# Kernel optimization log

Measured on AMD Instinct MI355X. Metric: run time of the kernel, lower is better.

Reference implementation:

```python
import jax, jax.numpy as jnp
import numpy as np

D = 512      # bit dimension
M = 131072   # stored reference points
B = 64       # query batch (batchLength in source)
EPS = 1e-6


def setup_inputs() -> dict:
    key = jax.random.key(0)
    k1, k2, k3, k4, k5 = jax.random.split(key, 5)
    return {
        "t_X1_T_bits": jax.random.randint(k1, (D, B), 0, 2, dtype=jnp.int32),
        "t_X2_T_bits": jax.random.randint(k2, (D, M), 0, 2, dtype=jnp.int32),
        # block-packed copy used only by the original custom backward; ignored here
        "t_X2_byDimBlock_T_bits": jax.random.randint(k3, (16, 1024), 0, 2, dtype=jnp.int32),
        "t_Y_knn": jax.random.normal(k4, (M,), dtype=jnp.float32),
        "t_W": jax.random.uniform(k5, (D,), dtype=jnp.float32, minval=0.5, maxval=1.5),
        "alpha": jnp.zeros((), jnp.float32),
        "beta": jnp.ones((), jnp.float32),
        "k": jnp.asarray(0.1, jnp.float32),
        "j": jnp.asarray(0.1, jnp.float32),
    }


def _squash_F(x, k, j):
    # F() from kNNFit: two-stage rational squash
    inner = x * (1 - k) / (k * (1 - 2 * jnp.abs(x)) + 1)
    t = 2 * inner - 1
    return 0.5 + 0.5 * t * (1 + j) / (-j * (1 - 2 * jnp.abs(t)) + 1)


def reference(t_X1_T_bits, t_X2_T_bits, t_X2_byDimBlock_T_bits, t_Y_knn,
              t_W, alpha, beta, k, j):
    # Weighted Hamming distance between every stored point (X2, [D,M]) and
    # every query (X1, [D,B]):
    #   WHD[m,b] = sum_d W[d] * (x1[d,b] XOR x2[d,m])
    # For 0/1 bits: xor = x1 + x2 - 2*x1*x2, so WHD decomposes into two
    # weighted bit-counts plus one GEMM (avoids a [D,M,B] intermediate).
    X1 = t_X1_T_bits.astype(jnp.float32)  # [D,B]
    X2 = t_X2_T_bits.astype(jnp.float32)  # [D,M]
    s1 = t_W @ X1                                            # [B]
    s2 = t_W @ X2                                            # [M]
    cross = jnp.einsum('dm,db->mb', X2, t_W[:, None] * X1)   # [M,B]
    t_WHDx = s1[None, :] + s2[:, None] - 2.0 * cross         # [M,B]

    t_norm_W = jnp.sum(jnp.abs(t_W)) + EPS                   # L1 norm
    t_FQx = _squash_F(1.0 - t_WHDx / t_norm_W, k, j)         # [M,B]
    t_score = jnp.mean(t_FQx * t_Y_knn[:, None], axis=0)     # [B]
    return beta * (t_score + alpha)
```

## Files before the change

kernel.cpp:

```cpp
#include <hip/hip_runtime.h>
#include <hip/hip_bf16.h>


#define DD 512
#define MM 131072
#define BQ 64
#define NWG 1024
#define NWAVES (NWG * 4)
#define WS_BFRAG 0
#define WS_META  65536
#define WS_PART  131072

typedef __attribute__((ext_vector_type(8))) short short8;
typedef __attribute__((ext_vector_type(16))) float floatx16;
typedef __attribute__((ext_vector_type(4))) unsigned int uintx4;
typedef __attribute__((ext_vector_type(4))) int intx4;

__global__ __launch_bounds__(256) void knn_setup(
    const int* __restrict__ X1, const float* __restrict__ W,
    void* __restrict__ ws) {
  short8* bm = (short8*)((char*)ws + WS_BFRAG);
  float* meta = (float*)((char*)ws + WS_META);
  const int tid = threadIdx.x;
#pragma unroll
  for (int i = 0; i < 16; ++i) {
    const int e = tid + 256 * i;
    const int lane = e & 63, t = (e >> 6) & 1, s = e >> 7;
    const int half = lane >> 5, col = lane & 31;
    const int b = t * 32 + col;
    short8 f;
#pragma unroll
    for (int j = 0; j < 8; ++j) {
      const int d = s * 16 + half * 8 + j;
      unsigned short hb = __builtin_bit_cast(unsigned short, __float2bfloat16(W[d]));
      if (X1[d * BQ + b]) hb ^= 0x8000u;
      f[j] = (short)hb;
    }
    bm[e] = f;
  }
  __shared__ float s1p[4][64];
  const int chunk = tid >> 6, b = tid & 63;
  float s = 0.f;
  for (int d = chunk * 128; d < chunk * 128 + 128; ++d)
    s += W[d] * (float)X1[d * BQ + b];
  s1p[chunk][b] = s;
  __syncthreads();
  if (tid < 64) {
    meta[tid] = s1p[0][tid] + s1p[1][tid] + s1p[2][tid] + s1p[3][tid];
    float nw = 0.f;
#pragma unroll
    for (int j = 0; j < 8; ++j) nw += fabsf(W[tid * 8 + j]);
    nw += __shfl_xor(nw, 32);
    nw += __shfl_xor(nw, 16);
    nw += __shfl_xor(nw, 8);
    nw += __shfl_xor(nw, 4);
    nw += __shfl_xor(nw, 2);
    nw += __shfl_xor(nw, 1);
    if (tid == 0) meta[64] = 1.0f / (nw + 1e-6f);
  }
}

__global__ __launch_bounds__(256, 4) void knn_main(
    const int* __restrict__ X2, const float* __restrict__ Y,
    const float* __restrict__ kp, const float* __restrict__ jp,
    const void* __restrict__ ws_ro, float* __restrict__ partials) {
  const short8* bm = (const short8*)((const char*)ws_ro + WS_BFRAG);
  const float* meta = (const float*)((const char*)ws_ro + WS_META);

  __shared__ __align__(16) unsigned int lds[4][2][320];

  const int tid = threadIdx.x;
  const int wv = tid >> 6, l = tid & 63;
  const int half = l >> 5, col = l & 31;
  const int m0 = blockIdx.x * 128 + wv * 32;
  unsigned int (*buf)[320] = lds[wv];

  const int r = l >> 3;
  const int mo = (l & 7) * 4;
  const int wbase = mo * 10 + r;
  const int rbase = col * 10 + half * 4;

  floatx16 acc0, acc1;
#pragma unroll
  for (int q = 0; q < 16; ++q) { acc0[q] = 0.f; acc1[q] = 0.f; }

  const int* g0 = X2 + (size_t)(2 * r) * MM + m0 + mo;

  intx4 ca, cb, na, nb;
  {
    const int* p = g0;
    ca = __builtin_nontemporal_load((const intx4*)p);
    cb = __builtin_nontemporal_load((const intx4*)(p + MM));
  }
#pragma unroll
  for (int i = 0; i < 4; ++i)
    buf[0][wbase + 10 * i] = (unsigned int)(ca[i] | (cb[i] << 16)) * 0x3F80u;
  {
    const int* p = g0 + (size_t)16 * MM;
    na = __builtin_nontemporal_load((const intx4*)p);
    nb = __builtin_nontemporal_load((const intx4*)(p + MM));
  }
  short8 bf0 = bm[0 * 64 + l];
  short8 bf1 = bm[1 * 64 + l];

#pragma unroll
  for (int s = 0; s < 32; ++s) {
    uint2 lo = *(const uint2*)&buf[s & 1][rbase];
    uint2 hi = *(const uint2*)&buf[s & 1][rbase + 2];
    uintx4 u;
    u[0] = lo.x; u[1] = lo.y; u[2] = hi.x; u[3] = hi.y;
    const short8 af = __builtin_bit_cast(short8, u);
    short8 nbf0 = bf0, nbf1 = bf1;
    if (s < 31) {
#pragma unroll
      for (int i = 0; i < 4; ++i)
        buf[(s + 1) & 1][wbase + 10 * i] =
            (unsigned int)(na[i] | (nb[i] << 16)) * 0x3F80u;
      nbf0 = bm[((s + 1) * 2 + 0) * 64 + l];
      nbf1 = bm[((s + 1) * 2 + 1) * 64 + l];
    }
    if (s < 30) {
      const int* p = g0 + (size_t)(s + 2) * 16 * MM;
      na = __builtin_nontemporal_load((const intx4*)p);
      nb = __builtin_nontemporal_load((const intx4*)(p + MM));
    }
    acc0 = __builtin_amdgcn_mfma_f32_32x32x16_bf16(af, bf0, acc0, 0, 0, 0);
    acc1 = __builtin_amdgcn_mfma_f32_32x32x16_bf16(af, bf1, acc1, 0, 0, 0);
    bf0 = nbf0; bf1 = nbf1;
  }

  const float inv_norm = meta[64];
  const float kk = kp[0], jj = jp[0];
  const float c1 = 1.0f - kk, c2 = 1.0f + jj;
  const float s1b0 = meta[col];
  const float s1b1 = meta[32 + col];
  float p0 = 0.f, p1 = 0.f;
#pragma unroll
  for (int q = 0; q < 16; ++q) {
    const int ml = (q & 3) + 8 * (q >> 2) + 4 * half;
    const float ym = Y[m0 + ml];
    {
      const float x = 1.0f - (s1b0 + acc0[q]) * inv_norm;
      const float inner = x * c1 / (kk * (1.0f - 2.0f * fabsf(x)) + 1.0f);
      const float t2 = 2.0f * inner - 1.0f;
      const float fq = 0.5f + 0.5f * t2 * c2 / (-jj * (1.0f - 2.0f * fabsf(t2)) + 1.0f);
      p0 += fq * ym;
    }
    {
      const float x = 1.0f - (s1b1 + acc1[q]) * inv_norm;
      const float inner = x * c1 / (kk * (1.0f - 2.0f * fabsf(x)) + 1.0f);
      const float t2 = 2.0f * inner - 1.0f;
      const float fq = 0.5f + 0.5f * t2 * c2 / (-jj * (1.0f - 2.0f * fabsf(t2)) + 1.0f);
      p1 += fq * ym;
    }
  }
  p0 += __shfl_xor(p0, 32);
  p1 += __shfl_xor(p1, 32);
  const int gw = blockIdx.x * 4 + wv;
  if (l < 32) {
    partials[(size_t)col * NWAVES + gw] = p0;
    partials[(size_t)(32 + col) * NWAVES + gw] = p1;
  }
}

__global__ __launch_bounds__(256) void knn_finalize(
    const float* __restrict__ partials, const float* __restrict__ alphap,
    const float* __restrict__ betap, float* __restrict__ out) {
  __shared__ float red[256];
  const int b = blockIdx.x, t = threadIdx.x;
  float s = 0.f;
#pragma unroll
  for (int i = 0; i < NWAVES / 256; ++i)
    s += partials[(size_t)b * NWAVES + i * 256 + t];
  red[t] = s;
  __syncthreads();
  if (t < 64) {
    float x = red[t] + red[t + 64] + red[t + 128] + red[t + 192];
    x += __shfl_xor(x, 32);
    x += __shfl_xor(x, 16);
    x += __shfl_xor(x, 8);
    x += __shfl_xor(x, 4);
    x += __shfl_xor(x, 2);
    x += __shfl_xor(x, 1);
    if (t == 0) out[b] = betap[0] * (x * (1.0f / (float)MM) + alphap[0]);
  }
}

extern "C" void kernel_launch(void* const* d_in, const int* in_sizes, int n_in,
                              void* d_out, int out_size, void* d_ws, size_t ws_size,
                              hipStream_t stream) {
  const int* X1 = (const int*)d_in[0];
  const int* X2 = (const int*)d_in[1];
  const float* Y = (const float*)d_in[3];
  const float* W = (const float*)d_in[4];
  const float* alphap = (const float*)d_in[5];
  const float* betap = (const float*)d_in[6];
  const float* kp = (const float*)d_in[7];
  const float* jp = (const float*)d_in[8];

  float* partials = (float*)((char*)d_ws + WS_PART);

  knn_setup<<<1, 256, 0, stream>>>(X1, W, d_ws);
  knn_main<<<NWG, 256, 0, stream>>>(X2, Y, kp, jp, d_ws, partials);
  knn_finalize<<<BQ, 256, 0, stream>>>(partials, alphap, betap, (float*)d_out);
}
```

Measured before the change: 384.1 us.

## Double per-wave M tile to 64 rows and parallelize setup across blocks

Each wave now computes a 64x64 output tile with four MFMA accumulators instead of 32x64, so each B-fragment load from the workspace is reused across two A tiles, and the grid shrinks to 512 workgroups with launch bounds lowered to 2 blocks per SIMD. The setup kernel is split across 17 blocks so the B-fragment packing and the s1/norm reduction run in parallel instead of in one serial block. The trade-off is higher register and LDS use per wave and fewer waves in flight to hide the X2 streaming latency on a bandwidth-bound kernel.

```diff
diff --git a/kernel.cpp b/kernel.cpp
--- a/kernel.cpp
+++ b/kernel.cpp
@@ -5,7 +5,8 @@
 #define DD 512
 #define MM 131072
 #define BQ 64
-#define NWG 1024
+#define MWG 256
+#define NWG (MM / MWG)
 #define NWAVES (NWG * 4)
 #define WS_BFRAG 0
 #define WS_META  65536
@@ -22,9 +23,9 @@
   short8* bm = (short8*)((char*)ws + WS_BFRAG);
   float* meta = (float*)((char*)ws + WS_META);
   const int tid = threadIdx.x;
-#pragma unroll
-  for (int i = 0; i < 16; ++i) {
-    const int e = tid + 256 * i;
+  const int bid = blockIdx.x;
+  if (bid < 16) {
+    const int e = bid * 256 + tid;
     const int lane = e & 63, t = (e >> 6) & 1, s = e >> 7;
     const int half = lane >> 5, col = lane & 31;
     const int b = t * 32 + col;
@@ -37,95 +38,115 @@
       f[j] = (short)hb;
     }
     bm[e] = f;
-  }
-  __shared__ float s1p[4][64];
-  const int chunk = tid >> 6, b = tid & 63;
-  float s = 0.f;
-  for (int d = chunk * 128; d < chunk * 128 + 128; ++d)
-    s += W[d] * (float)X1[d * BQ + b];
-  s1p[chunk][b] = s;
-  __syncthreads();
-  if (tid < 64) {
-    meta[tid] = s1p[0][tid] + s1p[1][tid] + s1p[2][tid] + s1p[3][tid];
-    float nw = 0.f;
-#pragma unroll
-    for (int j = 0; j < 8; ++j) nw += fabsf(W[tid * 8 + j]);
-    nw += __shfl_xor(nw, 32);
-    nw += __shfl_xor(nw, 16);
-    nw += __shfl_xor(nw, 8);
-    nw += __shfl_xor(nw, 4);
-    nw += __shfl_xor(nw, 2);
-    nw += __shfl_xor(nw, 1);
-    if (tid == 0) meta[64] = 1.0f / (nw + 1e-6f);
-  }
-}
-
-__global__ __launch_bounds__(256, 4) void knn_main(
+  } else {
+    __shared__ float s1p[4][64];
+    const int chunk = tid >> 6, b = tid & 63;
+    float s = 0.f;
+    for (int d = chunk * 128; d < chunk * 128 + 128; ++d)
+      s += W[d] * (float)X1[d * BQ + b];
+    s1p[chunk][b] = s;
+    __syncthreads();
+    if (tid < 64) {
+      meta[tid] = s1p[0][tid] + s1p[1][tid] + s1p[2][tid] + s1p[3][tid];
+      float nw = 0.f;
+#pragma unroll
+      for (int j = 0; j < 8; ++j) nw += fabsf(W[tid * 8 + j]);
+      nw += __shfl_xor(nw, 32);
+      nw += __shfl_xor(nw, 16);
+      nw += __shfl_xor(nw, 8);
+      nw += __shfl_xor(nw, 4);
+      nw += __shfl_xor(nw, 2);
+      nw += __shfl_xor(nw, 1);
+      if (tid == 0) meta[64] = 1.0f / (nw + 1e-6f);
+    }
+  }
+}
+
+__global__ __launch_bounds__(256, 2) void knn_main(
     const int* __restrict__ X2, const float* __restrict__ Y,
     const float* __restrict__ kp, const float* __restrict__ jp,
     const void* __restrict__ ws_ro, float* __restrict__ partials) {
   const short8* bm = (const short8*)((const char*)ws_ro + WS_BFRAG);
   const float* meta = (const float*)((const char*)ws_ro + WS_META);
 
-  __shared__ __align__(16) unsigned int lds[4][2][320];
+  __shared__ __align__(16) unsigned int lds[4][2][640];
 
   const int tid = threadIdx.x;
   const int wv = tid >> 6, l = tid & 63;
   const int half = l >> 5, col = l & 31;
-  const int m0 = blockIdx.x * 128 + wv * 32;
-  unsigned int (*buf)[320] = lds[wv];
+  const int m0 = blockIdx.x * MWG + wv * 64;
+  unsigned int (*buf)[640] = lds[wv];
 
   const int r = l >> 3;
   const int mo = (l & 7) * 4;
-  const int wbase = mo * 10 + r;
-  const int rbase = col * 10 + half * 4;
-
-  floatx16 acc0, acc1;
-#pragma unroll
-  for (int q = 0; q < 16; ++q) { acc0[q] = 0.f; acc1[q] = 0.f; }
+  const int wb0 = mo * 10 + r;
+  const int wb1 = (mo + 32) * 10 + r;
+  const int rb0 = col * 10 + half * 4;
+  const int rb1 = (col + 32) * 10 + half * 4;
+
+  floatx16 a00, a01, a10, a11;
+#pragma unroll
+  for (int q = 0; q < 16; ++q) { a00[q] = 0.f; a01[q] = 0.f; a10[q] = 0.f; a11[q] = 0.f; }
 
   const int* g0 = X2 + (size_t)(2 * r) * MM + m0 + mo;
 
-  intx4 ca, cb, na, nb;
+  intx4 c0a, c0b, c1a, c1b, n0a, n0b, n1a, n1b;
   {
     const int* p = g0;
-    ca = __builtin_nontemporal_load((const intx4*)p);
-    cb = __builtin_nontemporal_load((const intx4*)(p + MM));
-  }
-#pragma unroll
-  for (int i = 0; i < 4; ++i)
-    buf[0][wbase + 10 * i] = (unsigned int)(ca[i] | (cb[i] << 16)) * 0x3F80u;
+    c0a = __builtin_nontemporal_load((const intx4*)p);
+    c0b = __builtin_nontemporal_load((const intx4*)(p + MM));
+    c1a = __builtin_nontemporal_load((const intx4*)(p + 32));
+    c1b = __builtin_nontemporal_load((const intx4*)(p + MM + 32));
+  }
+#pragma unroll
+  for (int i = 0; i < 4; ++i) {
+    buf[0][wb0 + 10 * i] = (unsigned int)(c0a[i] | (c0b[i] << 16)) * 0x3F80u;
+    buf[0][wb1 + 10 * i] = (unsigned int)(c1a[i] | (c1b[i] << 16)) * 0x3F80u;
+  }
   {
     const int* p = g0 + (size_t)16 * MM;
-    na = __builtin_nontemporal_load((const intx4*)p);
-    nb = __builtin_nontemporal_load((const intx4*)(p + MM));
+    n0a = __builtin_nontemporal_load((const intx4*)p);
+    n0b = __builtin_nontemporal_load((const intx4*)(p + MM));
+    n1a = __builtin_nontemporal_load((const intx4*)(p + 32));
+    n1b = __builtin_nontemporal_load((const intx4*)(p + MM + 32));
   }
   short8 bf0 = bm[0 * 64 + l];
   short8 bf1 = bm[1 * 64 + l];
 
 #pragma unroll
   for (int s = 0; s < 32; ++s) {
-    uint2 lo = *(const uint2*)&buf[s & 1][rbase];
-    uint2 hi = *(const uint2*)&buf[s & 1][rbase + 2];
-    uintx4 u;
-    u[0] = lo.x; u[1] = lo.y; u[2] = hi.x; u[3] = hi.y;
-    const short8 af = __builtin_bit_cast(short8, u);
+    uintx4 u0, u1;
+    {
+      uint2 lo = *(const uint2*)&buf[s & 1][rb0];
+      uint2 hi = *(const uint2*)&buf[s & 1][rb0 + 2];
+      u0[0] = lo.x; u0[1] = lo.y; u0[2] = hi.x; u0[3] = hi.y;
+      lo = *(const uint2*)&buf[s & 1][rb1];
+      hi = *(const uint2*)&buf[s & 1][rb1 + 2];
+      u1[0] = lo.x; u1[1] = lo.y; u1[2] = hi.x; u1[3] = hi.y;
+    }
+    const short8 af0 = __builtin_bit_cast(short8, u0);
+    const short8 af1 = __builtin_bit_cast(short8, u1);
     short8 nbf0 = bf0, nbf1 = bf1;
     if (s < 31) {
 #pragma unroll
-      for (int i = 0; i < 4; ++i)
-        buf[(s + 1) & 1][wbase + 10 * i] =
-            (unsigned int)(na[i] | (nb[i] << 16)) * 0x3F80u;
+      for (int i = 0; i < 4; ++i) {
+        buf[(s + 1) & 1][wb0 + 10 * i] = (unsigned int)(n0a[i] | (n0b[i] << 16)) * 0x3F80u;
+        buf[(s + 1) & 1][wb1 + 10 * i] = (unsigned int)(n1a[i] | (n1b[i] << 16)) * 0x3F80u;
+      }
       nbf0 = bm[((s + 1) * 2 + 0) * 64 + l];
       nbf1 = bm[((s + 1) * 2 + 1) * 64 + l];
     }
     if (s < 30) {
       const int* p = g0 + (size_t)(s + 2) * 16 * MM;
-      na = __builtin_nontemporal_load((const intx4*)p);
-      nb = __builtin_nontemporal_load((const intx4*)(p + MM));
-    }
-    acc0 = __builtin_amdgcn_mfma_f32_32x32x16_bf16(af, bf0, acc0, 0, 0, 0);
-    acc1 = __builtin_amdgcn_mfma_f32_32x32x16_bf16(af, bf1, acc1, 0, 0, 0);
+      n0a = __builtin_nontemporal_load((const intx4*)p);
+      n0b = __builtin_nontemporal_load((const intx4*)(p + MM));
+      n1a = __builtin_nontemporal_load((const intx4*)(p + 32));
+      n1b = __builtin_nontemporal_load((const intx4*)(p + MM + 32));
+    }
+    a00 = __builtin_amdgcn_mfma_f32_32x32x16_bf16(af0, bf0, a00, 0, 0, 0);
+    a01 = __builtin_amdgcn_mfma_f32_32x32x16_bf16(af0, bf1, a01, 0, 0, 0);
+    a10 = __builtin_amdgcn_mfma_f32_32x32x16_bf16(af1, bf0, a10, 0, 0, 0);
+    a11 = __builtin_amdgcn_mfma_f32_32x32x16_bf16(af1, bf1, a11, 0, 0, 0);
     bf0 = nbf0; bf1 = nbf1;
   }
 
@@ -138,20 +159,35 @@
 #pragma unroll
   for (int q = 0; q < 16; ++q) {
     const int ml = (q & 3) + 8 * (q >> 2) + 4 * half;
-    const float ym = Y[m0 + ml];
-    {
-      const float x = 1.0f - (s1b0 + acc0[q]) * inv_norm;
-      const float inner = x * c1 / (kk * (1.0f - 2.0f * fabsf(x)) + 1.0f);
-      const float t2 = 2.0f * inner - 1.0f;
-      const float fq = 0.5f + 0.5f * t2 * c2 / (-jj * (1.0f - 2.0f * fabsf(t2)) + 1.0f);
-      p0 += fq * ym;
-    }
-    {
-      const float x = 1.0f - (s1b1 + acc1[q]) * inv_norm;
-      const float inner = x * c1 / (kk * (1.0f - 2.0f * fabsf(x)) + 1.0f);
-      const float t2 = 2.0f * inner - 1.0f;
-      const float fq = 0.5f + 0.5f * t2 * c2 / (-jj * (1.0f - 2.0f * fabsf(t2)) + 1.0f);
-      p1 += fq * ym;
+    const float ym0 = Y[m0 + ml];
+    const float ym1 = Y[m0 + 32 + ml];
+    {
+      const float x = 1.0f - (s1b0 + a00[q]) * inv_norm;
+      const float inner = x * c1 / (kk * (1.0f - 2.0f * fabsf(x)) + 1.0f);
+      const float t2 = 2.0f * inner - 1.0f;
+      const float fq = 0.5f + 0.5f * t2 * c2 / (-jj * (1.0f - 2.0f * fabsf(t2)) + 1.0f);
+      p0 += fq * ym0;
+    }
+    {
+      const float x = 1.0f - (s1b1 + a01[q]) * inv_norm;
+      const float inner = x * c1 / (kk * (1.0f - 2.0f * fabsf(x)) + 1.0f);
+      const float t2 = 2.0f * inner - 1.0f;
+      const float fq = 0.5f + 0.5f * t2 * c2 / (-jj * (1.0f - 2.0f * fabsf(t2)) + 1.0f);
+      p1 += fq * ym0;
+    }
+    {
+      const float x = 1.0f - (s1b0 + a10[q]) * inv_norm;
+      const float inner = x * c1 / (kk * (1.0f - 2.0f * fabsf(x)) + 1.0f);
+      const float t2 = 2.0f * inner - 1.0f;
+      const float fq = 0.5f + 0.5f * t2 * c2 / (-jj * (1.0f - 2.0f * fabsf(t2)) + 1.0f);
+      p0 += fq * ym1;
+    }
+    {
+      const float x = 1.0f - (s1b1 + a11[q]) * inv_norm;
+      const float inner = x * c1 / (kk * (1.0f - 2.0f * fabsf(x)) + 1.0f);
+      const float t2 = 2.0f * inner - 1.0f;
+      const float fq = 0.5f + 0.5f * t2 * c2 / (-jj * (1.0f - 2.0f * fabsf(t2)) + 1.0f);
+      p1 += fq * ym1;
     }
   }
   p0 += __shfl_xor(p0, 32);
@@ -200,7 +236,7 @@
 
   float* partials = (float*)((char*)d_ws + WS_PART);
 
-  knn_setup<<<1, 256, 0, stream>>>(X1, W, d_ws);
+  knn_setup<<<17, 256, 0, stream>>>(X1, W, d_ws);
   knn_main<<<NWG, 256, 0, stream>>>(X2, Y, kp, jp, d_ws, partials);
   knn_finalize<<<BQ, 256, 0, stream>>>(partials, alphap, betap, (float*)d_out);
 }
```

New measurement: 366.7 us. 4.5% less time.
